# Performance work log

Hardware: AMD Instinct MI355X
Metric: run time of the kernel (lower is better)

## Reference

```python
import jax, jax.numpy as jnp
import numpy as np

N_EMBED = 1024
HEAD_SIZE = 64
BLOCK_SIZE = 2048


def setup_inputs() -> dict:
    key = jax.random.key(0)
    kx, kk, kv = jax.random.split(key, 3)
    x = jax.random.normal(kx, (8, 2048, N_EMBED), dtype=jnp.float32)
    # nn.Linear(n_embed, head_size, bias=False): weight [head_size, n_embed]
    scale = 1.0 / np.sqrt(N_EMBED)
    W_k = jax.random.uniform(kk, (HEAD_SIZE, N_EMBED), dtype=jnp.float32, minval=-scale, maxval=scale)
    W_v = jax.random.uniform(kv, (HEAD_SIZE, N_EMBED), dtype=jnp.float32, minval=-scale, maxval=scale)
    return {"x": x, "W_k": W_k, "W_v": W_v}


def reference(x, W_k, W_v):
    # Faithful to source: q = self.key(x) (query projection is unused in the original forward)
    T = x.shape[1]
    k = jnp.einsum('btc,hc->bth', x, W_k)   # [B,T,H]
    q = k                                    # source bug: q uses key projection
    wei = jnp.einsum('bth,bsh->bts', q, k) * (HEAD_SIZE ** -0.5)  # [B,T,T]
    causal = jnp.tril(jnp.ones((T, T), dtype=bool))
    wei = jnp.where(causal, wei, -jnp.inf)
    wei = jax.nn.softmax(wei, axis=-1)
    v = jnp.einsum('btc,hc->bth', x, W_v)
    out = jnp.einsum('bts,bsh->bth', wei, v)
    return out
```

## Files before the change

### kernel.cpp

```cpp
#include <hip/hip_runtime.h>


typedef __bf16 bf16;
typedef __bf16 bf16x4 __attribute__((ext_vector_type(4)));
typedef __bf16 bf16x8 __attribute__((ext_vector_type(8)));
typedef float  floatx4 __attribute__((ext_vector_type(4)));

#define T_LEN 2048
#define HEAD  64
#define CEMB  1024

static __device__ __forceinline__ bf16x8 cvt2(float4 a, float4 b) {
    bf16x8 r;
    r[0] = (bf16)a.x; r[1] = (bf16)a.y; r[2] = (bf16)a.z; r[3] = (bf16)a.w;
    r[4] = (bf16)b.x; r[5] = (bf16)b.y; r[6] = (bf16)b.z; r[7] = (bf16)b.w;
    return r;
}

__global__ __launch_bounds__(256) void wconv_kernel(const float* __restrict__ Wk,
                                                    const float* __restrict__ Wv,
                                                    bf16* __restrict__ Wb) {
    int i = (blockIdx.x * 256 + threadIdx.x) * 4;
    const float* src = (i < 64 * 1024) ? (Wk + i) : (Wv + (i - 64 * 1024));
    float4 f = *(const float4*)src;
    bf16x4 v;
    v[0] = (bf16)f.x; v[1] = (bf16)f.y; v[2] = (bf16)f.z; v[3] = (bf16)f.w;
    *(bf16x4*)&Wb[i] = v;
}

__global__ __launch_bounds__(256) void proj_kernel(const float* __restrict__ x,
                                                   const bf16* __restrict__ Wb,
                                                   bf16* __restrict__ Kbuf,
                                                   bf16* __restrict__ Vt) {
    __shared__ __align__(16) bf16 As[2][32][72];
    __shared__ __align__(16) bf16 Bs[2][128][72];

    const int tid  = threadIdx.x;
    const int wave = tid >> 6;
    const int lane = tid & 63;
    const int quad = lane >> 4;
    const int low  = lane & 15;

    const long row0 = (long)blockIdx.x * 32;

    const int a_row = tid >> 3;
    const int a_col = (tid & 7) * 8;
    const int b_row = tid >> 1;
    const int b_col = (tid & 1) * 32;

    const float* abase = x + (row0 + a_row) * CEMB + a_col;
    const bf16*  bbase = Wb + b_row * CEMB + b_col;

    const int strip = wave & 1;
    const int nhalf = wave >> 1;
    const int nq    = nhalf * 4;

    floatx4 acc[4];
#pragma unroll
    for (int i = 0; i < 4; ++i) acc[i] = (floatx4){0.f, 0.f, 0.f, 0.f};

    float4 apf[2][2];
    bf16x8 bpf[2][4];

    apf[0][0] = ((const float4*)abase)[0];
    apf[0][1] = ((const float4*)abase)[1];
#pragma unroll
    for (int i = 0; i < 4; ++i) bpf[0][i] = *(const bf16x8*)(bbase + 8 * i);
    *(bf16x8*)&As[0][a_row][a_col] = cvt2(apf[0][0], apf[0][1]);
#pragma unroll
    for (int i = 0; i < 4; ++i) *(bf16x8*)&Bs[0][b_row][b_col + 8 * i] = bpf[0][i];
    apf[1][0] = ((const float4*)(abase + 64))[0];
    apf[1][1] = ((const float4*)(abase + 64))[1];
#pragma unroll
    for (int i = 0; i < 4; ++i) bpf[1][i] = *(const bf16x8*)(bbase + 64 + 8 * i);
    __syncthreads();

    int buf = 0;
    for (int s = 0; s < 16; ++s) {
        if (s < 15) {
            const int q  = (s + 1) & 1;
            const int nb = buf ^ 1;
            *(bf16x8*)&As[nb][a_row][a_col] = cvt2(apf[q][0], apf[q][1]);
#pragma unroll
            for (int i = 0; i < 4; ++i) *(bf16x8*)&Bs[nb][b_row][b_col + 8 * i] = bpf[q][i];
        }
        if (s < 14) {
            const int q  = s & 1;
            const int k0 = (s + 2) * 64;
            apf[q][0] = ((const float4*)(abase + k0))[0];
            apf[q][1] = ((const float4*)(abase + k0))[1];
#pragma unroll
            for (int i = 0; i < 4; ++i) bpf[q][i] = *(const bf16x8*)(bbase + k0 + 8 * i);
        }
#pragma unroll
        for (int ks = 0; ks < 2; ++ks) {
            bf16x8 afrag = *(const bf16x8*)&As[buf][strip * 16 + low][ks * 32 + quad * 8];
#pragma unroll
            for (int i = 0; i < 4; ++i) {
                bf16x8 bfrag = *(const bf16x8*)&Bs[buf][(nq + i) * 16 + low][ks * 32 + quad * 8];
                acc[i] = __builtin_amdgcn_mfma_f32_16x16x32_bf16(afrag, bfrag, acc[i], 0, 0, 0);
            }
        }
        if (s < 15) {
            __syncthreads();
            buf ^= 1;
        }
    }

    __syncthreads();
    bf16* Ek = (bf16*)&Bs[0][0][0];
    bf16* Ev = (bf16*)&Bs[1][0][0];
    if (nhalf == 0) {
#pragma unroll
        for (int i = 0; i < 4; ++i)
#pragma unroll
            for (int r = 0; r < 4; ++r)
                Ek[(strip * 16 + quad * 4 + r) * 72 + i * 16 + low] = (bf16)acc[i][r];
    } else {
#pragma unroll
        for (int i = 0; i < 4; ++i)
#pragma unroll
            for (int r = 0; r < 4; ++r)
                Ev[(i * 16 + low) * 36 + strip * 16 + quad * 4 + r] = (bf16)acc[i][r];
    }
    __syncthreads();

    const long bidx  = row0 >> 11;
    const int  tloc0 = (int)(row0 & 2047);
    {
        const int t  = tid >> 3;
        const int h0 = (tid & 7) * 8;
        *(bf16x8*)&Kbuf[(bidx * T_LEN + tloc0 + t) * HEAD + h0] = *(const bf16x8*)&Ek[t * 72 + h0];
    }
    {
        const int h  = tid >> 2;
        const int t0 = (tid & 3) * 8;
        *(bf16x8*)&Vt[(bidx * HEAD + h) * T_LEN + tloc0 + t0] = *(const bf16x8*)&Ev[h * 36 + t0];
    }
}

__global__ __launch_bounds__(256) void attn_kernel(const bf16* __restrict__ Kbuf,
                                                   const bf16* __restrict__ Vt,
                                                   bf16* __restrict__ Opart,
                                                   float* __restrict__ lpart) {
    __shared__ __align__(16) bf16 Ks[2][64][72];
    __shared__ __align__(16) bf16 Vs[2][64][72];
    __shared__ __align__(16) bf16 Ps[4][16][72];

    const int tid  = threadIdx.x;
    const int wave = tid >> 6;
    const int lane = tid & 63;
    const int quad = lane >> 4;
    const int low  = lane & 15;

    const int c  = blockIdx.x & 3;
    const int qb = (blockIdx.x >> 2) & 31;
    const int b  = blockIdx.x >> 7;

    const bf16* kbase = Kbuf + (long)b * T_LEN * HEAD;
    const bf16* vbase = Vt + (long)b * HEAD * T_LEN;

    const bf16* qrow = kbase + (qb * 64 + wave * 16 + low) * HEAD + quad * 8;
    const bf16x8 qf0 = *(const bf16x8*)(qrow);
    const bf16x8 qf1 = *(const bf16x8*)(qrow + 32);

    bf16x8 ones;
#pragma unroll
    for (int i = 0; i < 8; ++i) ones[i] = (bf16)1.0f;

    floatx4 o[4], ol;
#pragma unroll
    for (int nt = 0; nt < 4; ++nt) o[nt] = (floatx4){0.f, 0.f, 0.f, 0.f};
    ol = (floatx4){0.f, 0.f, 0.f, 0.f};

    const int s_row = tid >> 2;
    const int s_col = (tid & 3) * 16;
    const bf16* ksrc = kbase + s_row * HEAD + s_col;
    const bf16* vsrc = vbase + (long)s_row * T_LEN + s_col;

    if (c <= qb) {
        float4 kpf0 = *(const float4*)(ksrc + c * 4096);
        float4 kpf1 = *(const float4*)(ksrc + c * 4096 + 8);
        float4 vpf0 = *(const float4*)(vsrc + c * 64);
        float4 vpf1 = *(const float4*)(vsrc + c * 64 + 8);
        *(float4*)&Ks[0][s_row][s_col]     = kpf0;
        *(float4*)&Ks[0][s_row][s_col + 8] = kpf1;
        *(float4*)&Vs[0][s_row][s_col]     = vpf0;
        *(float4*)&Vs[0][s_row][s_col + 8] = vpf1;
        __syncthreads();

        int buf = 0;
        for (int j = c; j <= qb; j += 4) {
            const bool more = (j + 4 <= qb);
            if (more) {
                kpf0 = *(const float4*)(ksrc + (j + 4) * 4096);
                kpf1 = *(const float4*)(ksrc + (j + 4) * 4096 + 8);
                vpf0 = *(const float4*)(vsrc + (j + 4) * 64);
                vpf1 = *(const float4*)(vsrc + (j + 4) * 64 + 8);
            }

            floatx4 s_[4];
#pragma unroll
            for (int nt = 0; nt < 4; ++nt) {
                bf16x8 kf0 = *(const bf16x8*)&Ks[buf][nt * 16 + low][quad * 8];
                bf16x8 kf1 = *(const bf16x8*)&Ks[buf][nt * 16 + low][32 + quad * 8];
                floatx4 z = (floatx4){0.f, 0.f, 0.f, 0.f};
                z = __builtin_amdgcn_mfma_f32_16x16x32_bf16(qf0, kf0, z, 0, 0, 0);
                z = __builtin_amdgcn_mfma_f32_16x16x32_bf16(qf1, kf1, z, 0, 0, 0);
                s_[nt] = z;
            }

            const bool diag = (j == qb);
#pragma unroll
            for (int nt = 0; nt < 4; ++nt) {
#pragma unroll
                for (int r = 0; r < 4; ++r) {
                    float p = __builtin_amdgcn_exp2f(s_[nt][r] * 0.180336880f);
                    if (diag && (nt * 16 + low) > (wave * 16 + quad * 4 + r)) p = 0.f;
                    Ps[wave][quad * 4 + r][nt * 16 + low] = (bf16)p;
                }
            }

            bf16x8 pf0 = *(const bf16x8*)&Ps[wave][low][quad * 8];
            bf16x8 pf1 = *(const bf16x8*)&Ps[wave][low][32 + quad * 8];
#pragma unroll
            for (int nt = 0; nt < 4; ++nt) {
                bf16x8 vf0 = *(const bf16x8*)&Vs[buf][nt * 16 + low][quad * 8];
                bf16x8 vf1 = *(const bf16x8*)&Vs[buf][nt * 16 + low][32 + quad * 8];
                o[nt] = __builtin_amdgcn_mfma_f32_16x16x32_bf16(pf0, vf0, o[nt], 0, 0, 0);
                o[nt] = __builtin_amdgcn_mfma_f32_16x16x32_bf16(pf1, vf1, o[nt], 0, 0, 0);
            }
            ol = __builtin_amdgcn_mfma_f32_16x16x32_bf16(pf0, ones, ol, 0, 0, 0);
            ol = __builtin_amdgcn_mfma_f32_16x16x32_bf16(pf1, ones, ol, 0, 0, 0);

            if (more) {
                const int nb = buf ^ 1;
                *(float4*)&Ks[nb][s_row][s_col]     = kpf0;
                *(float4*)&Ks[nb][s_row][s_col + 8] = kpf1;
                *(float4*)&Vs[nb][s_row][s_col]     = vpf0;
                *(float4*)&Vs[nb][s_row][s_col + 8] = vpf1;
                __syncthreads();
                buf = nb;
            }
        }
    }

    __syncthreads();
    bf16* Eo = (bf16*)&Ks[0][0][0];
#pragma unroll
    for (int nt = 0; nt < 4; ++nt)
#pragma unroll
        for (int r = 0; r < 4; ++r)
            Eo[(wave * 16 + quad * 4 + r) * 72 + nt * 16 + low] = (bf16)o[nt][r];
    __syncthreads();
    {
        const int row  = tid >> 2;
        const int col0 = (tid & 3) * 16;
        bf16* ob = Opart + (long)blockIdx.x * 4096 + row * 64 + col0;
        *(bf16x8*)(ob)     = *(const bf16x8*)&Eo[row * 72 + col0];
        *(bf16x8*)(ob + 8) = *(const bf16x8*)&Eo[row * 72 + col0 + 8];
    }
    if (low == 0) {
#pragma unroll
        for (int r = 0; r < 4; ++r)
            lpart[(long)blockIdx.x * 64 + wave * 16 + quad * 4 + r] = ol[r];
    }
}

__global__ __launch_bounds__(256) void attn_combine(const bf16* __restrict__ Opart,
                                                    const float* __restrict__ lpart,
                                                    float* __restrict__ out) {
    const int tile = blockIdx.x;
    const int tid  = threadIdx.x;
    const int row  = tid >> 2;
    const int col0 = (tid & 3) * 16;

    const bf16*  ob = Opart + (long)tile * 4 * 4096 + row * 64 + col0;
    const float* lb = lpart + (long)tile * 4 * 64 + row;

    float l = lb[0] + lb[64] + lb[128] + lb[192];
    float rl = 1.0f / l;

    float s[16];
#pragma unroll
    for (int i = 0; i < 16; ++i) s[i] = 0.f;
#pragma unroll
    for (int ch = 0; ch < 4; ++ch) {
        bf16x8 u0 = *(const bf16x8*)(ob + ch * 4096);
        bf16x8 u1 = *(const bf16x8*)(ob + ch * 4096 + 8);
#pragma unroll
        for (int i = 0; i < 8; ++i) { s[i] += (float)u0[i]; s[8 + i] += (float)u1[i]; }
    }
    float4* op = (float4*)(out + (long)tile * 4096 + row * 64 + col0);
#pragma unroll
    for (int v = 0; v < 4; ++v) {
        float4 w;
        w.x = s[v * 4 + 0] * rl; w.y = s[v * 4 + 1] * rl;
        w.z = s[v * 4 + 2] * rl; w.w = s[v * 4 + 3] * rl;
        op[v] = w;
    }
}

extern "C" void kernel_launch(void* const* d_in, const int* in_sizes, int n_in,
                              void* d_out, int out_size, void* d_ws, size_t ws_size,
                              hipStream_t stream) {
    const float* x  = (const float*)d_in[0];
    const float* Wk = (const float*)d_in[1];
    const float* Wv = (const float*)d_in[2];
    float* out = (float*)d_out;

    char* ws = (char*)d_ws;
    bf16*  Wb    = (bf16*)ws;
    bf16*  Kbuf  = (bf16*)(ws + (1 << 20));
    bf16*  Vt    = (bf16*)(ws + (3 << 20));
    bf16*  Opart = (bf16*)(ws + (5 << 20));
    float* lpart = (float*)(ws + (13 << 20));

    wconv_kernel<<<128, 256, 0, stream>>>(Wk, Wv, Wb);
    proj_kernel<<<512, 256, 0, stream>>>(x, Wb, Kbuf, Vt);
    attn_kernel<<<1024, 256, 0, stream>>>(Kbuf, Vt, Opart, lpart);
    attn_combine<<<256, 256, 0, stream>>>(Opart, lpart, out);
}
```

Baseline: 129.4 us.

## Shrink projection row tile and give each attention block two query tiles

The projection kernel now handles 16 rows per block instead of 32, which doubles its grid to 1024 blocks, and each wave computes two N-tiles. The attention kernel now processes two 64-row query tiles per block (128 rows), so each K/V tile loaded into shared memory is reused for both query tiles. This halves the attention grid to 512 blocks and cuts K/V global traffic. In exchange it adds more registers per thread and a worse causal load balance, since the first query tile skips the last key tile. The combine kernel is remapped to the new partial layout.

```diff
diff --git a/kernel.cpp b/kernel.cpp
--- a/kernel.cpp
+++ b/kernel.cpp
@@ -14,6 +14,11 @@
     bf16x8 r;
     r[0] = (bf16)a.x; r[1] = (bf16)a.y; r[2] = (bf16)a.z; r[3] = (bf16)a.w;
     r[4] = (bf16)b.x; r[5] = (bf16)b.y; r[6] = (bf16)b.z; r[7] = (bf16)b.w;
+    return r;
+}
+static __device__ __forceinline__ bf16x4 cvt1(float4 a) {
+    bf16x4 r;
+    r[0] = (bf16)a.x; r[1] = (bf16)a.y; r[2] = (bf16)a.z; r[3] = (bf16)a.w;
     return r;
 }
 
@@ -23,17 +28,15 @@
     int i = (blockIdx.x * 256 + threadIdx.x) * 4;
     const float* src = (i < 64 * 1024) ? (Wk + i) : (Wv + (i - 64 * 1024));
     float4 f = *(const float4*)src;
-    bf16x4 v;
-    v[0] = (bf16)f.x; v[1] = (bf16)f.y; v[2] = (bf16)f.z; v[3] = (bf16)f.w;
-    *(bf16x4*)&Wb[i] = v;
+    *(bf16x4*)&Wb[i] = cvt1(f);
 }
 
 __global__ __launch_bounds__(256) void proj_kernel(const float* __restrict__ x,
                                                    const bf16* __restrict__ Wb,
                                                    bf16* __restrict__ Kbuf,
                                                    bf16* __restrict__ Vt) {
-    __shared__ __align__(16) bf16 As[2][32][72];
-    __shared__ __align__(16) bf16 Bs[2][128][72];
+    __shared__ __align__(16) bf16 As[2][16][72];
+    __shared__ __align__(16) bf16 Bs[2][128][68];
 
     const int tid  = threadIdx.x;
     const int wave = tid >> 6;
@@ -41,101 +44,94 @@
     const int quad = lane >> 4;
     const int low  = lane & 15;
 
-    const long row0 = (long)blockIdx.x * 32;
-
-    const int a_row = tid >> 3;
-    const int a_col = (tid & 7) * 8;
+    const long row0 = (long)blockIdx.x * 16;
+
+    const int a_row = tid >> 4;
+    const int a_col = (tid & 15) * 4;
     const int b_row = tid >> 1;
     const int b_col = (tid & 1) * 32;
 
     const float* abase = x + (row0 + a_row) * CEMB + a_col;
     const bf16*  bbase = Wb + b_row * CEMB + b_col;
 
-    const int strip = wave & 1;
-    const int nhalf = wave >> 1;
-    const int nq    = nhalf * 4;
-
-    floatx4 acc[4];
-#pragma unroll
-    for (int i = 0; i < 4; ++i) acc[i] = (floatx4){0.f, 0.f, 0.f, 0.f};
-
-    float4 apf[2][2];
+    const int nt0 = wave * 2;
+
+    floatx4 acc[2];
+    acc[0] = (floatx4){0.f, 0.f, 0.f, 0.f};
+    acc[1] = (floatx4){0.f, 0.f, 0.f, 0.f};
+
+    float4 apf[2];
     bf16x8 bpf[2][4];
 
-    apf[0][0] = ((const float4*)abase)[0];
-    apf[0][1] = ((const float4*)abase)[1];
+    apf[0] = *(const float4*)abase;
 #pragma unroll
     for (int i = 0; i < 4; ++i) bpf[0][i] = *(const bf16x8*)(bbase + 8 * i);
-    *(bf16x8*)&As[0][a_row][a_col] = cvt2(apf[0][0], apf[0][1]);
+    *(bf16x4*)&As[0][a_row][a_col] = cvt1(apf[0]);
 #pragma unroll
     for (int i = 0; i < 4; ++i) *(bf16x8*)&Bs[0][b_row][b_col + 8 * i] = bpf[0][i];
-    apf[1][0] = ((const float4*)(abase + 64))[0];
-    apf[1][1] = ((const float4*)(abase + 64))[1];
+    apf[1] = *(const float4*)(abase + 64);
 #pragma unroll
     for (int i = 0; i < 4; ++i) bpf[1][i] = *(const bf16x8*)(bbase + 64 + 8 * i);
     __syncthreads();
 
     int buf = 0;
     for (int s = 0; s < 16; ++s) {
-        if (s < 15) {
-            const int q  = (s + 1) & 1;
-            const int nb = buf ^ 1;
-            *(bf16x8*)&As[nb][a_row][a_col] = cvt2(apf[q][0], apf[q][1]);
-#pragma unroll
-            for (int i = 0; i < 4; ++i) *(bf16x8*)&Bs[nb][b_row][b_col + 8 * i] = bpf[q][i];
-        }
         if (s < 14) {
             const int q  = s & 1;
             const int k0 = (s + 2) * 64;
-            apf[q][0] = ((const float4*)(abase + k0))[0];
-            apf[q][1] = ((const float4*)(abase + k0))[1];
+            apf[q] = *(const float4*)(abase + k0);
 #pragma unroll
             for (int i = 0; i < 4; ++i) bpf[q][i] = *(const bf16x8*)(bbase + k0 + 8 * i);
         }
 #pragma unroll
         for (int ks = 0; ks < 2; ++ks) {
-            bf16x8 afrag = *(const bf16x8*)&As[buf][strip * 16 + low][ks * 32 + quad * 8];
-#pragma unroll
-            for (int i = 0; i < 4; ++i) {
-                bf16x8 bfrag = *(const bf16x8*)&Bs[buf][(nq + i) * 16 + low][ks * 32 + quad * 8];
+            bf16x8 afrag = *(const bf16x8*)&As[buf][low][ks * 32 + quad * 8];
+#pragma unroll
+            for (int i = 0; i < 2; ++i) {
+                bf16x8 bfrag = *(const bf16x8*)&Bs[buf][(nt0 + i) * 16 + low][ks * 32 + quad * 8];
                 acc[i] = __builtin_amdgcn_mfma_f32_16x16x32_bf16(afrag, bfrag, acc[i], 0, 0, 0);
             }
         }
         if (s < 15) {
+            const int q  = (s + 1) & 1;
+            const int nb = buf ^ 1;
+            *(bf16x4*)&As[nb][a_row][a_col] = cvt1(apf[q]);
+#pragma unroll
+            for (int i = 0; i < 4; ++i) *(bf16x8*)&Bs[nb][b_row][b_col + 8 * i] = bpf[q][i];
             __syncthreads();
-            buf ^= 1;
+            buf = nb;
         }
     }
 
     __syncthreads();
     bf16* Ek = (bf16*)&Bs[0][0][0];
     bf16* Ev = (bf16*)&Bs[1][0][0];
-    if (nhalf == 0) {
-#pragma unroll
-        for (int i = 0; i < 4; ++i)
+    if (wave < 2) {
+#pragma unroll
+        for (int i = 0; i < 2; ++i)
 #pragma unroll
             for (int r = 0; r < 4; ++r)
-                Ek[(strip * 16 + quad * 4 + r) * 72 + i * 16 + low] = (bf16)acc[i][r];
+                Ek[(quad * 4 + r) * 72 + wave * 32 + i * 16 + low] = (bf16)acc[i][r];
     } else {
 #pragma unroll
-        for (int i = 0; i < 4; ++i)
+        for (int i = 0; i < 2; ++i)
 #pragma unroll
             for (int r = 0; r < 4; ++r)
-                Ev[(i * 16 + low) * 36 + strip * 16 + quad * 4 + r] = (bf16)acc[i][r];
+                Ev[((wave - 2) * 32 + i * 16 + low) * 20 + quad * 4 + r] = (bf16)acc[i][r];
     }
     __syncthreads();
 
     const long bidx  = row0 >> 11;
     const int  tloc0 = (int)(row0 & 2047);
     {
-        const int t  = tid >> 3;
-        const int h0 = (tid & 7) * 8;
-        *(bf16x8*)&Kbuf[(bidx * T_LEN + tloc0 + t) * HEAD + h0] = *(const bf16x8*)&Ek[t * 72 + h0];
+        const int t  = tid >> 4;
+        const int h0 = (tid & 15) * 4;
+        *(bf16x4*)&Kbuf[(bidx * T_LEN + tloc0 + t) * HEAD + h0] = *(const bf16x4*)&Ek[t * 72 + h0];
     }
     {
         const int h  = tid >> 2;
-        const int t0 = (tid & 3) * 8;
-        *(bf16x8*)&Vt[(bidx * HEAD + h) * T_LEN + tloc0 + t0] = *(const bf16x8*)&Ev[h * 36 + t0];
+        const int t0 = (tid & 3) * 4;
+        *(bf16x4*)&Vt[(bidx * HEAD + h) * T_LEN + tloc0 + t0] = *(const bf16x4*)&Ev[h * 20 + t0];
     }
 }
 
@@ -145,7 +141,7 @@
                                                    float* __restrict__ lpart) {
     __shared__ __align__(16) bf16 Ks[2][64][72];
     __shared__ __align__(16) bf16 Vs[2][64][72];
-    __shared__ __align__(16) bf16 Ps[4][16][72];
+    __shared__ __align__(16) bf16 Ps[4][2][16][72];
 
     const int tid  = threadIdx.x;
     const int wave = tid >> 6;
@@ -154,31 +150,41 @@
     const int low  = lane & 15;
 
     const int c  = blockIdx.x & 3;
-    const int qb = (blockIdx.x >> 2) & 31;
-    const int b  = blockIdx.x >> 7;
+    const int qt = (blockIdx.x >> 2) & 15;
+    const int b  = blockIdx.x >> 6;
 
     const bf16* kbase = Kbuf + (long)b * T_LEN * HEAD;
     const bf16* vbase = Vt + (long)b * HEAD * T_LEN;
 
-    const bf16* qrow = kbase + (qb * 64 + wave * 16 + low) * HEAD + quad * 8;
-    const bf16x8 qf0 = *(const bf16x8*)(qrow);
-    const bf16x8 qf1 = *(const bf16x8*)(qrow + 32);
+    bf16x8 qf[2][2];
+#pragma unroll
+    for (int t = 0; t < 2; ++t) {
+        const bf16* qrow = kbase + (qt * 128 + t * 64 + wave * 16 + low) * HEAD + quad * 8;
+        qf[t][0] = *(const bf16x8*)(qrow);
+        qf[t][1] = *(const bf16x8*)(qrow + 32);
+    }
 
     bf16x8 ones;
 #pragma unroll
     for (int i = 0; i < 8; ++i) ones[i] = (bf16)1.0f;
 
-    floatx4 o[4], ol;
-#pragma unroll
-    for (int nt = 0; nt < 4; ++nt) o[nt] = (floatx4){0.f, 0.f, 0.f, 0.f};
-    ol = (floatx4){0.f, 0.f, 0.f, 0.f};
+    floatx4 o[2][4], ol[2];
+#pragma unroll
+    for (int t = 0; t < 2; ++t) {
+#pragma unroll
+        for (int nt = 0; nt < 4; ++nt) o[t][nt] = (floatx4){0.f, 0.f, 0.f, 0.f};
+        ol[t] = (floatx4){0.f, 0.f, 0.f, 0.f};
+    }
+
+    const int jmax = 2 * qt + 1;
+    const int jd0  = 2 * qt;
 
     const int s_row = tid >> 2;
     const int s_col = (tid & 3) * 16;
     const bf16* ksrc = kbase + s_row * HEAD + s_col;
     const bf16* vsrc = vbase + (long)s_row * T_LEN + s_col;
 
-    if (c <= qb) {
+    if (c <= jmax) {
         float4 kpf0 = *(const float4*)(ksrc + c * 4096);
         float4 kpf1 = *(const float4*)(ksrc + c * 4096 + 8);
         float4 vpf0 = *(const float4*)(vsrc + c * 64);
@@ -190,8 +196,8 @@
         __syncthreads();
 
         int buf = 0;
-        for (int j = c; j <= qb; j += 4) {
-            const bool more = (j + 4 <= qb);
+        for (int j = c; j <= jmax; j += 4) {
+            const bool more = (j + 4 <= jmax);
             if (more) {
                 kpf0 = *(const float4*)(ksrc + (j + 4) * 4096);
                 kpf1 = *(const float4*)(ksrc + (j + 4) * 4096 + 8);
@@ -199,39 +205,41 @@
                 vpf1 = *(const float4*)(vsrc + (j + 4) * 64 + 8);
             }
 
-            floatx4 s_[4];
-#pragma unroll
-            for (int nt = 0; nt < 4; ++nt) {
-                bf16x8 kf0 = *(const bf16x8*)&Ks[buf][nt * 16 + low][quad * 8];
-                bf16x8 kf1 = *(const bf16x8*)&Ks[buf][nt * 16 + low][32 + quad * 8];
-                floatx4 z = (floatx4){0.f, 0.f, 0.f, 0.f};
-                z = __builtin_amdgcn_mfma_f32_16x16x32_bf16(qf0, kf0, z, 0, 0, 0);
-                z = __builtin_amdgcn_mfma_f32_16x16x32_bf16(qf1, kf1, z, 0, 0, 0);
-                s_[nt] = z;
+#pragma unroll
+            for (int t = 0; t < 2; ++t) {
+                if (t == 0 && j > jd0) continue;
+                floatx4 s_[4];
+#pragma unroll
+                for (int nt = 0; nt < 4; ++nt) {
+                    bf16x8 kf0 = *(const bf16x8*)&Ks[buf][nt * 16 + low][quad * 8];
+                    bf16x8 kf1 = *(const bf16x8*)&Ks[buf][nt * 16 + low][32 + quad * 8];
+                    floatx4 z = (floatx4){0.f, 0.f, 0.f, 0.f};
+                    z = __builtin_amdgcn_mfma_f32_16x16x32_bf16(qf[t][0], kf0, z, 0, 0, 0);
+                    z = __builtin_amdgcn_mfma_f32_16x16x32_bf16(qf[t][1], kf1, z, 0, 0, 0);
+                    s_[nt] = z;
+                }
+                const bool diag = (j == jd0 + t);
+#pragma unroll
+                for (int nt = 0; nt < 4; ++nt) {
+#pragma unroll
+                    for (int r = 0; r < 4; ++r) {
+                        float p = __builtin_amdgcn_exp2f(s_[nt][r] * 0.180336880f);
+                        if (diag && (nt * 16 + low) > (wave * 16 + quad * 4 + r)) p = 0.f;
+                        Ps[wave][t][quad * 4 + r][nt * 16 + low] = (bf16)p;
+                    }
+                }
+                bf16x8 pf0 = *(const bf16x8*)&Ps[wave][t][low][quad * 8];
+                bf16x8 pf1 = *(const bf16x8*)&Ps[wave][t][low][32 + quad * 8];
+#pragma unroll
+                for (int nt = 0; nt < 4; ++nt) {
+                    bf16x8 vf0 = *(const bf16x8*)&Vs[buf][nt * 16 + low][quad * 8];
+                    bf16x8 vf1 = *(const bf16x8*)&Vs[buf][nt * 16 + low][32 + quad * 8];
+                    o[t][nt] = __builtin_amdgcn_mfma_f32_16x16x32_bf16(pf0, vf0, o[t][nt], 0, 0, 0);
+                    o[t][nt] = __builtin_amdgcn_mfma_f32_16x16x32_bf16(pf1, vf1, o[t][nt], 0, 0, 0);
+                }
+                ol[t] = __builtin_amdgcn_mfma_f32_16x16x32_bf16(pf0, ones, ol[t], 0, 0, 0);
+                ol[t] = __builtin_amdgcn_mfma_f32_16x16x32_bf16(pf1, ones, ol[t], 0, 0, 0);
             }
-
-            const bool diag = (j == qb);
-#pragma unroll
-            for (int nt = 0; nt < 4; ++nt) {
-#pragma unroll
-                for (int r = 0; r < 4; ++r) {
-                    float p = __builtin_amdgcn_exp2f(s_[nt][r] * 0.180336880f);
-                    if (diag && (nt * 16 + low) > (wave * 16 + quad * 4 + r)) p = 0.f;
-                    Ps[wave][quad * 4 + r][nt * 16 + low] = (bf16)p;
-                }
-            }
-
-            bf16x8 pf0 = *(const bf16x8*)&Ps[wave][low][quad * 8];
-            bf16x8 pf1 = *(const bf16x8*)&Ps[wave][low][32 + quad * 8];
-#pragma unroll
-            for (int nt = 0; nt < 4; ++nt) {
-                bf16x8 vf0 = *(const bf16x8*)&Vs[buf][nt * 16 + low][quad * 8];
-                bf16x8 vf1 = *(const bf16x8*)&Vs[buf][nt * 16 + low][32 + quad * 8];
-                o[nt] = __builtin_amdgcn_mfma_f32_16x16x32_bf16(pf0, vf0, o[nt], 0, 0, 0);
-                o[nt] = __builtin_amdgcn_mfma_f32_16x16x32_bf16(pf1, vf1, o[nt], 0, 0, 0);
-            }
-            ol = __builtin_amdgcn_mfma_f32_16x16x32_bf16(pf0, ones, ol, 0, 0, 0);
-            ol = __builtin_amdgcn_mfma_f32_16x16x32_bf16(pf1, ones, ol, 0, 0, 0);
 
             if (more) {
                 const int nb = buf ^ 1;
@@ -248,37 +256,48 @@
     __syncthreads();
     bf16* Eo = (bf16*)&Ks[0][0][0];
 #pragma unroll
-    for (int nt = 0; nt < 4; ++nt)
-#pragma unroll
-        for (int r = 0; r < 4; ++r)
-            Eo[(wave * 16 + quad * 4 + r) * 72 + nt * 16 + low] = (bf16)o[nt][r];
+    for (int t = 0; t < 2; ++t)
+#pragma unroll
+        for (int nt = 0; nt < 4; ++nt)
+#pragma unroll
+            for (int r = 0; r < 4; ++r)
+                Eo[(t * 64 + wave * 16 + quad * 4 + r) * 72 + nt * 16 + low] = (bf16)o[t][nt][r];
     __syncthreads();
     {
-        const int row  = tid >> 2;
-        const int col0 = (tid & 3) * 16;
-        bf16* ob = Opart + (long)blockIdx.x * 4096 + row * 64 + col0;
-        *(bf16x8*)(ob)     = *(const bf16x8*)&Eo[row * 72 + col0];
-        *(bf16x8*)(ob + 8) = *(const bf16x8*)&Eo[row * 72 + col0 + 8];
+        const int row  = tid >> 1;
+        const int col0 = (tid & 1) * 32;
+        bf16* ob = Opart + (long)blockIdx.x * 8192 + row * 64 + col0;
+#pragma unroll
+        for (int i = 0; i < 4; ++i)
+            *(bf16x8*)(ob + 8 * i) = *(const bf16x8*)&Eo[row * 72 + col0 + 8 * i];
     }
     if (low == 0) {
 #pragma unroll
-        for (int r = 0; r < 4; ++r)
-            lpart[(long)blockIdx.x * 64 + wave * 16 + quad * 4 + r] = ol[r];
+        for (int t = 0; t < 2; ++t)
+#pragma unroll
+            for (int r = 0; r < 4; ++r)
+                lpart[(long)blockIdx.x * 128 + t * 64 + wave * 16 + quad * 4 + r] = ol[t][r];
     }
 }
 
 __global__ __launch_bounds__(256) void attn_combine(const bf16* __restrict__ Opart,
                                                     const float* __restrict__ lpart,
                                                     float* __restrict__ out) {
-    const int tile = blockIdx.x;
+    const int g    = blockIdx.x;
+    const int b    = g >> 5;
+    const int t64  = g & 31;
+    const int qt   = t64 >> 1;
+    const int half = t64 & 1;
     const int tid  = threadIdx.x;
     const int row  = tid >> 2;
     const int col0 = (tid & 3) * 16;
 
-    const bf16*  ob = Opart + (long)tile * 4 * 4096 + row * 64 + col0;
-    const float* lb = lpart + (long)tile * 4 * 64 + row;
-
-    float l = lb[0] + lb[64] + lb[128] + lb[192];
+    const long blk0 = ((long)(b * 16 + qt)) * 4;
+    const int  lrow = half * 64 + row;
+
+    float l = 0.f;
+#pragma unroll
+    for (int ch = 0; ch < 4; ++ch) l += lpart[(blk0 + ch) * 128 + lrow];
     float rl = 1.0f / l;
 
     float s[16];
@@ -286,12 +305,13 @@
     for (int i = 0; i < 16; ++i) s[i] = 0.f;
 #pragma unroll
     for (int ch = 0; ch < 4; ++ch) {
-        bf16x8 u0 = *(const bf16x8*)(ob + ch * 4096);
-        bf16x8 u1 = *(const bf16x8*)(ob + ch * 4096 + 8);
+        const bf16* ob = Opart + (blk0 + ch) * 8192 + lrow * 64 + col0;
+        bf16x8 u0 = *(const bf16x8*)(ob);
+        bf16x8 u1 = *(const bf16x8*)(ob + 8);
 #pragma unroll
         for (int i = 0; i < 8; ++i) { s[i] += (float)u0[i]; s[8 + i] += (float)u1[i]; }
     }
-    float4* op = (float4*)(out + (long)tile * 4096 + row * 64 + col0);
+    float4* op = (float4*)(out + ((long)b * T_LEN + t64 * 64 + row) * HEAD + col0);
 #pragma unroll
     for (int v = 0; v < 4; ++v) {
         float4 w;
@@ -317,7 +337,7 @@
     float* lpart = (float*)(ws + (13 << 20));
 
     wconv_kernel<<<128, 256, 0, stream>>>(Wk, Wv, Wb);
-    proj_kernel<<<512, 256, 0, stream>>>(x, Wb, Kbuf, Vt);
-    attn_kernel<<<1024, 256, 0, stream>>>(Kbuf, Vt, Opart, lpart);
+    proj_kernel<<<1024, 256, 0, stream>>>(x, Wb, Kbuf, Vt);
+    attn_kernel<<<512, 256, 0, stream>>>(Kbuf, Vt, Opart, lpart);
     attn_combine<<<256, 256, 0, stream>>>(Opart, lpart, out);
 }
```

New measurement: 141.9 us. +9.6%, slower.

## Stage projection and attention tiles via async global-to-LDS loads with XOR swizzle

Applied to the files above, without the earlier changes.

Both the projection and the attention kernels now use global_load_lds (direct global-to-shared DMA) instead of loading into registers and then writing to LDS. The padded shared tiles are replaced by unpadded tiles with an XOR-swizzled column layout to avoid bank conflicts. In the projection kernel, x is now kept as fp32 in LDS and converted to bf16 when each fragment is read, which doubles the A-tile footprint. The aim is to cut register pressure and VALU/LDS-store instructions in the prefetch path. The risk is relying on barriers to cover completion of the async loads, plus the larger LDS use in the projection kernel.

```diff
diff --git a/kernel.cpp b/kernel.cpp
--- a/kernel.cpp
+++ b/kernel.cpp
@@ -9,6 +9,12 @@
 #define T_LEN 2048
 #define HEAD  64
 #define CEMB  1024
+
+static __device__ __forceinline__ void async16(const void* g, void* l) {
+    __builtin_amdgcn_global_load_lds(
+        (const __attribute__((address_space(1))) void*)g,
+        (__attribute__((address_space(3))) void*)l, 16, 0, 0);
+}
 
 static __device__ __forceinline__ bf16x8 cvt2(float4 a, float4 b) {
     bf16x8 r;
@@ -16,24 +22,26 @@
     r[4] = (bf16)b.x; r[5] = (bf16)b.y; r[6] = (bf16)b.z; r[7] = (bf16)b.w;
     return r;
 }
+static __device__ __forceinline__ bf16x4 cvt1(float4 a) {
+    bf16x4 r;
+    r[0] = (bf16)a.x; r[1] = (bf16)a.y; r[2] = (bf16)a.z; r[3] = (bf16)a.w;
+    return r;
+}
 
 __global__ __launch_bounds__(256) void wconv_kernel(const float* __restrict__ Wk,
                                                     const float* __restrict__ Wv,
                                                     bf16* __restrict__ Wb) {
     int i = (blockIdx.x * 256 + threadIdx.x) * 4;
     const float* src = (i < 64 * 1024) ? (Wk + i) : (Wv + (i - 64 * 1024));
-    float4 f = *(const float4*)src;
-    bf16x4 v;
-    v[0] = (bf16)f.x; v[1] = (bf16)f.y; v[2] = (bf16)f.z; v[3] = (bf16)f.w;
-    *(bf16x4*)&Wb[i] = v;
+    *(bf16x4*)&Wb[i] = cvt1(*(const float4*)src);
 }
 
 __global__ __launch_bounds__(256) void proj_kernel(const float* __restrict__ x,
                                                    const bf16* __restrict__ Wb,
                                                    bf16* __restrict__ Kbuf,
                                                    bf16* __restrict__ Vt) {
-    __shared__ __align__(16) bf16 As[2][32][72];
-    __shared__ __align__(16) bf16 Bs[2][128][72];
+    __shared__ __align__(16) float As[2][32 * 64];
+    __shared__ __align__(16) bf16  Bs[2][128 * 64];
 
     const int tid  = threadIdx.x;
     const int wave = tid >> 6;
@@ -43,74 +51,64 @@
 
     const long row0 = (long)blockIdx.x * 32;
 
-    const int a_row = tid >> 3;
-    const int a_col = (tid & 7) * 8;
-    const int b_row = tid >> 1;
-    const int b_col = (tid & 1) * 32;
-
-    const float* abase = x + (row0 + a_row) * CEMB + a_col;
-    const bf16*  bbase = Wb + b_row * CEMB + b_col;
+    const int ar_ = lane >> 4;
+    const int ac_ = (lane & 15) ^ (wave * 4 + ar_);
+    const int br_ = lane >> 3;
+    const int bc_ = (lane & 7) ^ br_;
 
     const int strip = wave & 1;
-    const int nhalf = wave >> 1;
-    const int nq    = nhalf * 4;
+    const int nq    = (wave >> 1) * 4;
 
     floatx4 acc[4];
 #pragma unroll
     for (int i = 0; i < 4; ++i) acc[i] = (floatx4){0.f, 0.f, 0.f, 0.f};
 
-    float4 apf[2][2];
-    bf16x8 bpf[2][4];
-
-    apf[0][0] = ((const float4*)abase)[0];
-    apf[0][1] = ((const float4*)abase)[1];
-#pragma unroll
-    for (int i = 0; i < 4; ++i) bpf[0][i] = *(const bf16x8*)(bbase + 8 * i);
-    *(bf16x8*)&As[0][a_row][a_col] = cvt2(apf[0][0], apf[0][1]);
-#pragma unroll
-    for (int i = 0; i < 4; ++i) *(bf16x8*)&Bs[0][b_row][b_col + 8 * i] = bpf[0][i];
-    apf[1][0] = ((const float4*)(abase + 64))[0];
-    apf[1][1] = ((const float4*)(abase + 64))[1];
-#pragma unroll
-    for (int i = 0; i < 4; ++i) bpf[1][i] = *(const bf16x8*)(bbase + 64 + 8 * i);
+    auto stage = [&](int s, int sb) {
+        const int k0 = s * 64;
+#pragma unroll
+        for (int m = 0; m < 2; ++m) {
+            const int r = (m * 4 + wave) * 4 + ar_;
+            async16(x + (row0 + r) * CEMB + k0 + ac_ * 4, &As[sb][(m * 4 + wave) * 256]);
+        }
+#pragma unroll
+        for (int m = 0; m < 4; ++m) {
+            const int r = (m * 4 + wave) * 8 + br_;
+            async16(Wb + r * CEMB + k0 + bc_ * 8, &Bs[sb][(m * 4 + wave) * 512]);
+        }
+    };
+
+    stage(0, 0);
+    stage(1, 1);
     __syncthreads();
 
     int buf = 0;
     for (int s = 0; s < 16; ++s) {
-        if (s < 15) {
-            const int q  = (s + 1) & 1;
-            const int nb = buf ^ 1;
-            *(bf16x8*)&As[nb][a_row][a_col] = cvt2(apf[q][0], apf[q][1]);
-#pragma unroll
-            for (int i = 0; i < 4; ++i) *(bf16x8*)&Bs[nb][b_row][b_col + 8 * i] = bpf[q][i];
-        }
-        if (s < 14) {
-            const int q  = s & 1;
-            const int k0 = (s + 2) * 64;
-            apf[q][0] = ((const float4*)(abase + k0))[0];
-            apf[q][1] = ((const float4*)(abase + k0))[1];
-#pragma unroll
-            for (int i = 0; i < 4; ++i) bpf[q][i] = *(const bf16x8*)(bbase + k0 + 8 * i);
-        }
 #pragma unroll
         for (int ks = 0; ks < 2; ++ks) {
-            bf16x8 afrag = *(const bf16x8*)&As[buf][strip * 16 + low][ks * 32 + quad * 8];
+            const int rr = strip * 16 + low;
+            const int c0 = ks * 8 + quad * 2;
+            float4 a0 = *(const float4*)&As[buf][rr * 64 + ((c0 ^ low) * 4)];
+            float4 a1 = *(const float4*)&As[buf][rr * 64 + (((c0 + 1) ^ low) * 4)];
+            bf16x8 afrag = cvt2(a0, a1);
+            const int cq = ks * 4 + quad;
 #pragma unroll
             for (int i = 0; i < 4; ++i) {
-                bf16x8 bfrag = *(const bf16x8*)&Bs[buf][(nq + i) * 16 + low][ks * 32 + quad * 8];
+                const int r2 = (nq + i) * 16 + low;
+                bf16x8 bfrag = *(const bf16x8*)&Bs[buf][r2 * 64 + ((cq ^ (low & 7)) * 8)];
                 acc[i] = __builtin_amdgcn_mfma_f32_16x16x32_bf16(afrag, bfrag, acc[i], 0, 0, 0);
             }
         }
         if (s < 15) {
             __syncthreads();
+            if (s < 14) stage(s + 2, buf);
             buf ^= 1;
         }
     }
 
     __syncthreads();
-    bf16* Ek = (bf16*)&Bs[0][0][0];
-    bf16* Ev = (bf16*)&Bs[1][0][0];
-    if (nhalf == 0) {
+    bf16* Ek = (bf16*)&Bs[0][0];
+    bf16* Ev = (bf16*)&Bs[1][0];
+    if (wave < 2) {
 #pragma unroll
         for (int i = 0; i < 4; ++i)
 #pragma unroll
@@ -143,8 +141,8 @@
                                                    const bf16* __restrict__ Vt,
                                                    bf16* __restrict__ Opart,
                                                    float* __restrict__ lpart) {
-    __shared__ __align__(16) bf16 Ks[2][64][72];
-    __shared__ __align__(16) bf16 Vs[2][64][72];
+    __shared__ __align__(16) bf16 Ks[2][64 * 64];
+    __shared__ __align__(16) bf16 Vs[2][64 * 64];
     __shared__ __align__(16) bf16 Ps[4][16][72];
 
     const int tid  = threadIdx.x;
@@ -173,37 +171,31 @@
     for (int nt = 0; nt < 4; ++nt) o[nt] = (floatx4){0.f, 0.f, 0.f, 0.f};
     ol = (floatx4){0.f, 0.f, 0.f, 0.f};
 
-    const int s_row = tid >> 2;
-    const int s_col = (tid & 3) * 16;
-    const bf16* ksrc = kbase + s_row * HEAD + s_col;
-    const bf16* vsrc = vbase + (long)s_row * T_LEN + s_col;
+    const int br_ = lane >> 3;
+    const int bc_ = (lane & 7) ^ br_;
+
+    auto stage = [&](int j, int sb) {
+#pragma unroll
+        for (int m = 0; m < 2; ++m) {
+            const int r = (m * 4 + wave) * 8 + br_;
+            async16(kbase + (j * 64 + r) * HEAD + bc_ * 8, &Ks[sb][(m * 4 + wave) * 512]);
+            async16(vbase + (long)r * T_LEN + j * 64 + bc_ * 8, &Vs[sb][(m * 4 + wave) * 512]);
+        }
+    };
 
     if (c <= qb) {
-        float4 kpf0 = *(const float4*)(ksrc + c * 4096);
-        float4 kpf1 = *(const float4*)(ksrc + c * 4096 + 8);
-        float4 vpf0 = *(const float4*)(vsrc + c * 64);
-        float4 vpf1 = *(const float4*)(vsrc + c * 64 + 8);
-        *(float4*)&Ks[0][s_row][s_col]     = kpf0;
-        *(float4*)&Ks[0][s_row][s_col + 8] = kpf1;
-        *(float4*)&Vs[0][s_row][s_col]     = vpf0;
-        *(float4*)&Vs[0][s_row][s_col + 8] = vpf1;
+        stage(c, 0);
+        if (c + 4 <= qb) stage(c + 4, 1);
         __syncthreads();
 
         int buf = 0;
         for (int j = c; j <= qb; j += 4) {
-            const bool more = (j + 4 <= qb);
-            if (more) {
-                kpf0 = *(const float4*)(ksrc + (j + 4) * 4096);
-                kpf1 = *(const float4*)(ksrc + (j + 4) * 4096 + 8);
-                vpf0 = *(const float4*)(vsrc + (j + 4) * 64);
-                vpf1 = *(const float4*)(vsrc + (j + 4) * 64 + 8);
-            }
-
             floatx4 s_[4];
 #pragma unroll
             for (int nt = 0; nt < 4; ++nt) {
-                bf16x8 kf0 = *(const bf16x8*)&Ks[buf][nt * 16 + low][quad * 8];
-                bf16x8 kf1 = *(const bf16x8*)&Ks[buf][nt * 16 + low][32 + quad * 8];
+                const int r2 = nt * 16 + low;
+                bf16x8 kf0 = *(const bf16x8*)&Ks[buf][r2 * 64 + ((quad ^ (low & 7)) * 8)];
+                bf16x8 kf1 = *(const bf16x8*)&Ks[buf][r2 * 64 + (((4 + quad) ^ (low & 7)) * 8)];
                 floatx4 z = (floatx4){0.f, 0.f, 0.f, 0.f};
                 z = __builtin_amdgcn_mfma_f32_16x16x32_bf16(qf0, kf0, z, 0, 0, 0);
                 z = __builtin_amdgcn_mfma_f32_16x16x32_bf16(qf1, kf1, z, 0, 0, 0);
@@ -225,28 +217,25 @@
             bf16x8 pf1 = *(const bf16x8*)&Ps[wave][low][32 + quad * 8];
 #pragma unroll
             for (int nt = 0; nt < 4; ++nt) {
-                bf16x8 vf0 = *(const bf16x8*)&Vs[buf][nt * 16 + low][quad * 8];
-                bf16x8 vf1 = *(const bf16x8*)&Vs[buf][nt * 16 + low][32 + quad * 8];
+                const int r2 = nt * 16 + low;
+                bf16x8 vf0 = *(const bf16x8*)&Vs[buf][r2 * 64 + ((quad ^ (low & 7)) * 8)];
+                bf16x8 vf1 = *(const bf16x8*)&Vs[buf][r2 * 64 + (((4 + quad) ^ (low & 7)) * 8)];
                 o[nt] = __builtin_amdgcn_mfma_f32_16x16x32_bf16(pf0, vf0, o[nt], 0, 0, 0);
                 o[nt] = __builtin_amdgcn_mfma_f32_16x16x32_bf16(pf1, vf1, o[nt], 0, 0, 0);
             }
             ol = __builtin_amdgcn_mfma_f32_16x16x32_bf16(pf0, ones, ol, 0, 0, 0);
             ol = __builtin_amdgcn_mfma_f32_16x16x32_bf16(pf1, ones, ol, 0, 0, 0);
 
-            if (more) {
-                const int nb = buf ^ 1;
-                *(float4*)&Ks[nb][s_row][s_col]     = kpf0;
-                *(float4*)&Ks[nb][s_row][s_col + 8] = kpf1;
-                *(float4*)&Vs[nb][s_row][s_col]     = vpf0;
-                *(float4*)&Vs[nb][s_row][s_col + 8] = vpf1;
+            if (j + 4 <= qb) {
                 __syncthreads();
-                buf = nb;
-            }
-        }
-    }
-
-    __syncthreads();
-    bf16* Eo = (bf16*)&Ks[0][0][0];
+                if (j + 8 <= qb) stage(j + 8, buf);
+                buf ^= 1;
+            }
+        }
+    }
+
+    __syncthreads();
+    bf16* Eo = (bf16*)&Ks[0][0];
 #pragma unroll
     for (int nt = 0; nt < 4; ++nt)
 #pragma unroll
```

Result: no change. 131.3 us (+1.4%).
